# Kernel tuning notes

Measured on AMD Instinct MI355X. Metric: run time of the kernel, lower is better.

Reference implementation:

```python
import jax, jax.numpy as jnp
import numpy as np

BEAMS = 2
DEPTH = 3
NEXP = 4
HID = 128
NCLS = 100
EPS = 1e-5


def _conv(x, w, b):
    y = jax.lax.conv_general_dilated(x, w, (1, 1), 'VALID',
                                     dimension_numbers=('NCHW', 'OIHW', 'NCHW'))
    return y + b.reshape(1, -1, 1, 1)


def _bn(x, g, b):
    # training-mode batch norm over (N, H, W) per channel
    m = jnp.mean(x, axis=(0, 2, 3), keepdims=True)
    v = jnp.var(x, axis=(0, 2, 3), keepdims=True)
    return (x - m) * jax.lax.rsqrt(v + EPS) * g.reshape(1, -1, 1, 1) + b.reshape(1, -1, 1, 1)


def _pool(x):
    return jax.lax.reduce_window(x, 0.0, jax.lax.add, (1, 1, 2, 2), (1, 1, 2, 2), 'VALID') * 0.25


def _backbone(x, blocks):
    h = x
    for (w, b, g, bb) in blocks:  # 3 fixed conv blocks
        h = _pool(jax.nn.relu(_bn(_conv(h, w, b), g, bb)))
    return h.reshape(h.shape[0], -1)  # [B, 128]


def _routed_mlp(h, trajectories, expert_W, expert_b):
    # h: [N, 128] with N = B*BEAMS; trajectories: [DEPTH, B, BEAMS, NEXP]
    N = h.shape[0]
    for d in range(DEPTH):
        ops = trajectories[d].reshape(N, NEXP)
        sel = jnp.argmax(ops, axis=1)                              # per-sample expert id
        all_out = jnp.einsum('nd,eod->neo', h, expert_W) + expert_b[None]  # [N, NEXP, 128]
        out = jnp.take_along_axis(all_out, sel[:, None, None], axis=1)[:, 0, :]
        mx = jnp.max(ops, axis=1, keepdims=True)
        out = out + mx - jax.lax.stop_gradient(mx)                 # straight-through router tie
        if d != DEPTH - 1:
            out = jax.nn.relu(out)
        h = out
    return h


def setup_inputs() -> dict:
    key = jax.random.key(0)
    ks = jax.random.split(key, 12)
    B = 2048
    x = jax.random.normal(ks[0], (B, 3, 32, 32), jnp.float32)
    trajectories = jax.random.uniform(ks[1], (DEPTH, B, BEAMS, NEXP), jnp.float32)
    score_values = jax.random.normal(ks[2], (B, BEAMS), jnp.float32)
    # conv blocks
    cw1 = jax.random.normal(ks[3], (32, 3, 3, 3), jnp.float32) * 0.1
    cb1 = jnp.zeros((32,), jnp.float32)
    g1 = jnp.ones((32,), jnp.float32)
    bb1 = jnp.zeros((32,), jnp.float32)
    cw2 = jax.random.normal(ks[4], (32, 32, 3, 3), jnp.float32) * 0.06
    cb2 = jnp.zeros((32,), jnp.float32)
    g2 = jnp.ones((32,), jnp.float32)
    bb2 = jnp.zeros((32,), jnp.float32)
    cw3 = jax.random.normal(ks[5], (32, 32, 3, 3), jnp.float32) * 0.06
    cb3 = jnp.zeros((32,), jnp.float32)
    g3 = jnp.ones((32,), jnp.float32)
    bb3 = jnp.zeros((32,), jnp.float32)
    # experts: 3 Linear(128,128) + Identity (eye weight, zero bias)
    eW = jax.random.normal(ks[6], (3, HID, HID), jnp.float32) * 0.05
    expert_W = jnp.concatenate([eW, jnp.eye(HID, dtype=jnp.float32)[None]], axis=0)  # [4,128,128]
    eb = jax.random.normal(ks[7], (3, HID), jnp.float32) * 0.01
    expert_b = jnp.concatenate([eb, jnp.zeros((1, HID), jnp.float32)], axis=0)       # [4,128]
    out_W = jax.random.normal(ks[8], (NCLS, HID), jnp.float32) * 0.05
    out_b = jnp.zeros((NCLS,), jnp.float32)
    return dict(x=x, trajectories=trajectories, score_values=score_values,
                cw1=cw1, cb1=cb1, g1=g1, bb1=bb1,
                cw2=cw2, cb2=cb2, g2=g2, bb2=bb2,
                cw3=cw3, cb3=cb3, g3=g3, bb3=bb3,
                expert_W=expert_W, expert_b=expert_b, out_W=out_W, out_b=out_b)


def reference(x, trajectories, score_values,
              cw1, cb1, g1, bb1, cw2, cb2, g2, bb2, cw3, cb3, g3, bb3,
              expert_W, expert_b, out_W, out_b):
    blocks = [(cw1, cb1, g1, bb1), (cw2, cb2, g2, bb2), (cw3, cb3, g3, bb3)]
    h0 = _backbone(x, blocks)                       # [B, 128]
    h = jnp.repeat(h0, BEAMS, axis=0)               # [B*BEAMS, 128], sample-major like torch expand+view
    h = _routed_mlp(h, trajectories, expert_W, expert_b)
    preds = h @ out_W.T + out_b                     # [B*BEAMS, 100]
    logp = jax.nn.log_softmax(preds, axis=1)
    return (logp, score_values)
```

## Files before the change

### kernel.cpp

```cpp
#include <hip/hip_runtime.h>
#include <math.h>

typedef unsigned short us;
typedef short s16x8 __attribute__((ext_vector_type(8)));
typedef float f32x4 __attribute__((ext_vector_type(4)));

#define EPSV 1e-5f

static __device__ inline us f2bf(float f) {
  union { float f; unsigned u; } v; v.f = f;
  unsigned r = v.u + 0x7fffu + ((v.u >> 16) & 1u);
  return (us)(r >> 16);
}
static __device__ inline unsigned cvtpk(float lo, float hi) {
  unsigned r;
  asm("v_cvt_pk_bf16_f32 %0, %1, %2" : "=v"(r) : "v"(lo), "v"(hi));
  return r;
}
static __device__ inline us f2bf1(float f) { return (us)cvtpk(f, 0.f); }
static __device__ inline float bflo(unsigned u) { return __uint_as_float(u << 16); }
static __device__ inline float bfhi(unsigned u) { return __uint_as_float(u & 0xffff0000u); }

union AU { s16x8 v; us e[8]; };

__global__ __launch_bounds__(256) void prep_weights(
    const float* __restrict__ w1, const float* __restrict__ w2,
    const float* __restrict__ w3, const float* __restrict__ eW,
    const float* __restrict__ oW,
    us* __restrict__ wt1L, us* __restrict__ wt1Lb,
    us* __restrict__ wt2L, us* __restrict__ wt3L,
    us* __restrict__ ewB, us* __restrict__ owB) {
  const int gtid = blockIdx.x * 256 + threadIdx.x;
  const int G = gridDim.x * 256;
  for (int i = gtid; i < 1280; i += G) {
    const int oc = i / 40, k = i % 40, t = k >> 2, c = k & 3;
    wt1L[i] = (t < 9 && c < 3) ? f2bf(w1[oc * 27 + c * 9 + t]) : (us)0;
    wt1Lb[i] = (k < 3) ? f2bf(w1[oc * 27 + k * 9 + 8]) : (us)0;
  }
  for (int i = gtid; i < 11520; i += G) {
    const int row = i / 40, col = i % 40;
    const int tap = row >> 5, oc = row & 31;
    wt2L[i] = (col < 32) ? f2bf(w2[oc * 288 + col * 9 + tap]) : (us)0;
    wt3L[i] = (col < 32) ? f2bf(w3[oc * 288 + col * 9 + tap]) : (us)0;
  }
  for (int i = gtid; i < 49152; i += G) ewB[i] = f2bf(eW[i]);
  for (int i = gtid; i < 14336; i += G) {
    const int cls = i >> 7;
    owB[i] = (cls < 100) ? f2bf(oW[cls * 128 + (i & 127)]) : (us)0;
  }
}

__global__ __launch_bounds__(256) void finalize_stats(
    const float* __restrict__ part, const float* __restrict__ g,
    const float* __restrict__ bb, float cnt, float* __restrict__ stats) {
  __shared__ float redS[256], redQ[256];
  const int ch = blockIdx.x, tid = threadIdx.x;
  const float* ps = part + (size_t)ch * 2048;
  const float* pq = part + (size_t)(32 + ch) * 2048;
  float s = 0.f, q = 0.f;
  for (int i = tid; i < 2048; i += 256) { s += ps[i]; q += pq[i]; }
  redS[tid] = s; redQ[tid] = q;
  __syncthreads();
  for (int off = 128; off; off >>= 1) {
    if (tid < off) { redS[tid] += redS[tid + off]; redQ[tid] += redQ[tid + off]; }
    __syncthreads();
  }
  if (tid == 0) {
    const float mean = redS[0] / cnt;
    const float var = redQ[0] / cnt - mean * mean;
    const float sc = g[ch] * rsqrtf(var + EPSV);
    stats[ch] = sc;
    stats[32 + ch] = bb[ch] - mean * sc;
  }
}

static __device__ inline void stage_x_cminor(const float* xp, us* xsb4, int tid) {
#pragma unroll
  for (int k = 0; k < 4; ++k) {
    const int p = tid + k * 256;
    const unsigned lo = cvtpk(xp[p], xp[1024 + p]);
    const unsigned hi = cvtpk(xp[2048 + p], 0.f);
    *(uint2*)&xsb4[p * 4] = make_uint2(lo, hi);
  }
}

static __device__ inline void build_tbl1(us* tbl, int tid) {
  for (int i = tid; i < 928; i += 256) {
    us v = 0;
    if (i < 900) {
      const int w = i >> 2, e = i & 3;
      v = (us)((((2 * (w / 15) + (e >> 1)) * 32 + 2 * (w % 15) + (e & 1))) * 4);
    }
    tbl[i] = v;
  }
}

__global__ __launch_bounds__(256, 4) void conv1_stats(
    const float* __restrict__ x, const us* __restrict__ wt1L,
    const us* __restrict__ wt1Lb, const float* __restrict__ cb,
    float* __restrict__ part1) {
  __shared__ __align__(16) us xsb4[4096];
  __shared__ us tbl1[928];
  __shared__ float csum[32], css[32];
  const int n = blockIdx.x, tid = threadIdx.x;
  const int wave = tid >> 6, lane = tid & 63, row16 = lane & 15, kg = lane >> 4;
  stage_x_cminor(x + (size_t)n * 3072, xsb4, tid);
  build_tbl1(tbl1, tid);
  if (tid < 32) { csum[tid] = 0.f; css[tid] = 0.f; }
  __syncthreads();
  const int t0 = 2 * kg, t1 = 2 * kg + 1;
  const int toff0 = ((t0 / 3) * 32 + t0 % 3) * 4;
  const int toff1 = ((t1 / 3) * 32 + t1 % 3) * 4;
  const s16x8 wf0 = *(const s16x8*)&wt1L[row16 * 40 + kg * 8];
  const s16x8 wf1 = *(const s16x8*)&wt1L[(16 + row16) * 40 + kg * 8];
  const s16x8 wb0 = *(const s16x8*)&wt1Lb[row16 * 40 + kg * 8];
  const s16x8 wb1 = *(const s16x8*)&wt1Lb[(16 + row16) * 40 + kg * 8];
  const float bias0 = cb[row16], bias1 = cb[16 + row16];
  AU a2;
#pragma unroll
  for (int j = 0; j < 8; ++j) a2.e[j] = 0;
  float s0 = 0.f, ss0 = 0.f, s1 = 0.f, ss1 = 0.f;
  for (int mt = wave; mt < 57; mt += 4) {
    const int pixA = mt * 16 + row16;
    const int boff = tbl1[pixA];
    AU a;
    *(uint2*)&a.e[0] = *(const uint2*)&xsb4[boff + toff0];
    *(uint2*)&a.e[4] = *(const uint2*)&xsb4[boff + toff1];
    if (kg == 0) *(uint2*)&a2.e[0] = *(const uint2*)&xsb4[boff + 264];
    f32x4 acc0 = {bias0, bias0, bias0, bias0};
    f32x4 acc1 = {bias1, bias1, bias1, bias1};
    acc0 = __builtin_amdgcn_mfma_f32_16x16x32_bf16(a.v, wf0, acc0, 0, 0, 0);
    acc0 = __builtin_amdgcn_mfma_f32_16x16x32_bf16(a2.v, wb0, acc0, 0, 0, 0);
    acc1 = __builtin_amdgcn_mfma_f32_16x16x32_bf16(a.v, wf1, acc1, 0, 0, 0);
    acc1 = __builtin_amdgcn_mfma_f32_16x16x32_bf16(a2.v, wb1, acc1, 0, 0, 0);
#pragma unroll
    for (int r = 0; r < 4; ++r) {
      const int pix = mt * 16 + kg * 4 + r;
      if (pix < 900) {
        s0 += acc0[r]; ss0 += acc0[r] * acc0[r];
        s1 += acc1[r]; ss1 += acc1[r] * acc1[r];
      }
    }
  }
  s0 += __shfl_down(s0, 32); s0 += __shfl_down(s0, 16);
  ss0 += __shfl_down(ss0, 32); ss0 += __shfl_down(ss0, 16);
  s1 += __shfl_down(s1, 32); s1 += __shfl_down(s1, 16);
  ss1 += __shfl_down(ss1, 32); ss1 += __shfl_down(ss1, 16);
  if (lane < 16) {
    atomicAdd(&csum[row16], s0); atomicAdd(&css[row16], ss0);
    atomicAdd(&csum[16 + row16], s1); atomicAdd(&css[16 + row16], ss1);
  }
  __syncthreads();
  if (tid < 32) {
    part1[tid * 2048 + n] = csum[tid];
    part1[(32 + tid) * 2048 + n] = css[tid];
  }
}

__global__ __launch_bounds__(256, 4) void conv1_apply_conv2_stats(
    const float* __restrict__ x, const us* __restrict__ wt1L,
    const us* __restrict__ wt1Lb, const float* __restrict__ cb1,
    const float* __restrict__ stats1,
    const us* __restrict__ wt2L, const float* __restrict__ cb2,
    float* __restrict__ part2, us* __restrict__ y2s) {
  __shared__ __align__(16) us xsb4[4096];
  __shared__ __align__(16) us p1b[9000];
  __shared__ us tbl1[928];
  __shared__ us tbl2[176];
  __shared__ float scS[32], shS[32], csum[32], css[32];
  const int n = blockIdx.x, tid = threadIdx.x;
  const int wave = tid >> 6, lane = tid & 63, row16 = lane & 15, kg = lane >> 4;
  stage_x_cminor(x + (size_t)n * 3072, xsb4, tid);
  build_tbl1(tbl1, tid);
  if (tid < 176) {
    us v = 0;
    const int q = tid;
    if (q < 144) {
      const int w = q >> 2, e = q & 3;
      v = (us)((2 * (w / 6) + (e >> 1)) * 15 + 2 * (w % 6) + (e & 1));
    } else if (q < 169) {
      const int r = q - 144;
      v = (us)((r < 13) ? (12 * 15 + r) : ((r - 13) * 15 + 12));
    }
    tbl2[tid] = v;
  }
  if (tid < 32) {
    scS[tid] = stats1[tid]; shS[tid] = stats1[32 + tid];
    csum[tid] = 0.f; css[tid] = 0.f;
  }
  __syncthreads();
  {
    const int t0 = 2 * kg, t1 = 2 * kg + 1;
    const int toff0 = ((t0 / 3) * 32 + t0 % 3) * 4;
    const int toff1 = ((t1 / 3) * 32 + t1 % 3) * 4;
    const s16x8 wf0 = *(const s16x8*)&wt1L[row16 * 40 + kg * 8];
    const s16x8 wf1 = *(const s16x8*)&wt1L[(16 + row16) * 40 + kg * 8];
    const s16x8 wb0 = *(const s16x8*)&wt1Lb[row16 * 40 + kg * 8];
    const s16x8 wb1 = *(const s16x8*)&wt1Lb[(16 + row16) * 40 + kg * 8];
    const float bias0 = cb1[row16], bias1 = cb1[16 + row16];
    const float sc0 = scS[row16], sh0 = shS[row16];
    const float sc1 = scS[16 + row16], sh1 = shS[16 + row16];
    AU a2;
#pragma unroll
    for (int j = 0; j < 8; ++j) a2.e[j] = 0;
    for (int mt = wave; mt < 57; mt += 4) {
      const int pixA = mt * 16 + row16;
      const int boff = tbl1[pixA];
      AU a;
      *(uint2*)&a.e[0] = *(const uint2*)&xsb4[boff + toff0];
      *(uint2*)&a.e[4] = *(const uint2*)&xsb4[boff + toff1];
      if (kg == 0) *(uint2*)&a2.e[0] = *(const uint2*)&xsb4[boff + 264];
      f32x4 acc0 = {bias0, bias0, bias0, bias0};
      f32x4 acc1 = {bias1, bias1, bias1, bias1};
      acc0 = __builtin_amdgcn_mfma_f32_16x16x32_bf16(a.v, wf0, acc0, 0, 0, 0);
      acc0 = __builtin_amdgcn_mfma_f32_16x16x32_bf16(a2.v, wb0, acc0, 0, 0, 0);
      acc1 = __builtin_amdgcn_mfma_f32_16x16x32_bf16(a.v, wf1, acc1, 0, 0, 0);
      acc1 = __builtin_amdgcn_mfma_f32_16x16x32_bf16(a2.v, wb1, acc1, 0, 0, 0);
      const int w = mt * 4 + kg;
      if (w < 225) {
        float p0 = 0.f, p1v = 0.f;
#pragma unroll
        for (int r = 0; r < 4; ++r) {
          p0 += fmaxf(acc0[r] * sc0 + sh0, 0.f);
          p1v += fmaxf(acc1[r] * sc1 + sh1, 0.f);
        }
        p1b[w * 40 + row16] = f2bf1(p0 * 0.25f);
        p1b[w * 40 + 16 + row16] = f2bf1(p1v * 0.25f);
      }
    }
  }
  __syncthreads();
  int inb[3], mtv[3];
#pragma unroll
  for (int m = 0; m < 3; ++m) {
    const int mt = wave + 4 * m;
    mtv[m] = mt;
    const int q = mt * 16 + row16;
    inb[m] = tbl2[(q < 176) ? q : 0];
  }
  const float b20 = cb2[row16], b21 = cb2[16 + row16];
  f32x4 acc[3][2];
#pragma unroll
  for (int m = 0; m < 3; ++m) {
    acc[m][0] = {b20, b20, b20, b20};
    acc[m][1] = {b21, b21, b21, b21};
  }
#pragma unroll
  for (int tap = 0; tap < 9; ++tap) {
    const int ki = tap / 3, kj = tap % 3;
    const s16x8 wf0 = *(const s16x8*)&wt2L[(tap * 32 + row16) * 40 + kg * 8];
    const s16x8 wf1 = *(const s16x8*)&wt2L[(tap * 32 + 16 + row16) * 40 + kg * 8];
#pragma unroll
    for (int m = 0; m < 3; ++m) {
      if (mtv[m] < 11) {
        const s16x8 a = *(const s16x8*)&p1b[(inb[m] + ki * 15 + kj) * 40 + kg * 8];
        acc[m][0] = __builtin_amdgcn_mfma_f32_16x16x32_bf16(a, wf0, acc[m][0], 0, 0, 0);
        acc[m][1] = __builtin_amdgcn_mfma_f32_16x16x32_bf16(a, wf1, acc[m][1], 0, 0, 0);
      }
    }
  }
  float s0 = 0.f, ss0 = 0.f, s1 = 0.f, ss1 = 0.f;
#pragma unroll
  for (int m = 0; m < 3; ++m) {
    if (mtv[m] < 11) {
      if (mtv[m] < 9) {
        const int w = mtv[m] * 4 + kg;
        uint2 pk0, pk1;
        pk0.x = cvtpk(acc[m][0][0], acc[m][0][1]);
        pk0.y = cvtpk(acc[m][0][2], acc[m][0][3]);
        pk1.x = cvtpk(acc[m][1][0], acc[m][1][1]);
        pk1.y = cvtpk(acc[m][1][2], acc[m][1][3]);
        *(uint2*)(y2s + (((size_t)n * 36 + w) * 32 + row16) * 4) = pk0;
        *(uint2*)(y2s + (((size_t)n * 36 + w) * 32 + 16 + row16) * 4) = pk1;
      }
#pragma unroll
      for (int r = 0; r < 4; ++r) {
        const int q = mtv[m] * 16 + kg * 4 + r;
        if (q < 169) {
          const float u0 = acc[m][0][r], u1 = acc[m][1][r];
          s0 += u0; ss0 += u0 * u0; s1 += u1; ss1 += u1 * u1;
        }
      }
    }
  }
  s0 += __shfl_down(s0, 32); s0 += __shfl_down(s0, 16);
  ss0 += __shfl_down(ss0, 32); ss0 += __shfl_down(ss0, 16);
  s1 += __shfl_down(s1, 32); s1 += __shfl_down(s1, 16);
  ss1 += __shfl_down(ss1, 32); ss1 += __shfl_down(ss1, 16);
  if (lane < 16) {
    atomicAdd(&csum[row16], s0); atomicAdd(&css[row16], ss0);
    atomicAdd(&csum[16 + row16], s1); atomicAdd(&css[16 + row16], ss1);
  }
  __syncthreads();
  if (tid < 32) {
    part2[tid * 2048 + n] = csum[tid];
    part2[(32 + tid) * 2048 + n] = css[tid];
  }
}

__global__ __launch_bounds__(256) void bnpool2_conv3_stats(
    const us* __restrict__ y2s, const float* __restrict__ stats2,
    const us* __restrict__ wt3L, const float* __restrict__ cb3,
    float* __restrict__ part3, us* __restrict__ p2g) {
  __shared__ __align__(16) us p2L[11520];
  __shared__ float scS[32], shS[32], csum[32], css[32];
  const int n0 = blockIdx.x * 8, tid = threadIdx.x;
  const int wave = tid >> 6, lane = tid & 63, row16 = lane & 15, kg = lane >> 4;
  if (tid < 32) {
    scS[tid] = stats2[tid]; shS[tid] = stats2[32 + tid];
    csum[tid] = 0.f; css[tid] = 0.f;
  }
  __syncthreads();
#pragma unroll
  for (int it = 0; it < 36; ++it) {
    const int i = tid + it * 256;
    const int c = i & 31, w = (i >> 5) % 36, s = i / 1152;
    const uint2 v = *(const uint2*)(y2s + (((size_t)(n0 + s) * 36 + w) * 32 + c) * 4);
    const float sc = scS[c], sh = shS[c];
    const float p = fmaxf(bflo(v.x) * sc + sh, 0.f) + fmaxf(bfhi(v.x) * sc + sh, 0.f) +
                    fmaxf(bflo(v.y) * sc + sh, 0.f) + fmaxf(bfhi(v.y) * sc + sh, 0.f);
    const us pb = f2bf1(p * 0.25f);
    p2L[(s * 36 + w) * 40 + c] = pb;
    p2g[((size_t)(n0 + s) * 36 + w) * 32 + c] = pb;
  }
  __syncthreads();
  const int inb3 = (row16 >> 2) * 6 + (row16 & 3);
  const float b30 = cb3[row16], b31 = cb3[16 + row16];
  float s0 = 0.f, ss0 = 0.f, s1 = 0.f, ss1 = 0.f;
#pragma unroll
  for (int si = 0; si < 2; ++si) {
    const int s = wave * 2 + si;
    f32x4 a0 = {b30, b30, b30, b30};
    f32x4 a1 = {b31, b31, b31, b31};
#pragma unroll
    for (int tap = 0; tap < 9; ++tap) {
      const int ki = tap / 3, kj = tap % 3;
      const s16x8 wf0 = *(const s16x8*)&wt3L[(tap * 32 + row16) * 40 + kg * 8];
      const s16x8 wf1 = *(const s16x8*)&wt3L[(tap * 32 + 16 + row16) * 40 + kg * 8];
      const s16x8 a = *(const s16x8*)&p2L[(s * 36 + inb3 + ki * 6 + kj) * 40 + kg * 8];
      a0 = __builtin_amdgcn_mfma_f32_16x16x32_bf16(a, wf0, a0, 0, 0, 0);
      a1 = __builtin_amdgcn_mfma_f32_16x16x32_bf16(a, wf1, a1, 0, 0, 0);
    }
#pragma unroll
    for (int r = 0; r < 4; ++r) {
      s0 += a0[r]; ss0 += a0[r] * a0[r];
      s1 += a1[r]; ss1 += a1[r] * a1[r];
    }
  }
  s0 += __shfl_down(s0, 32); s0 += __shfl_down(s0, 16);
  ss0 += __shfl_down(ss0, 32); ss0 += __shfl_down(ss0, 16);
  s1 += __shfl_down(s1, 32); s1 += __shfl_down(s1, 16);
  ss1 += __shfl_down(ss1, 32); ss1 += __shfl_down(ss1, 16);
  if (lane < 16) {
    atomicAdd(&csum[row16], s0); atomicAdd(&css[row16], ss0);
    atomicAdd(&csum[16 + row16], s1); atomicAdd(&css[16 + row16], ss1);
  }
  __syncthreads();
  if (tid < 32) {
    part3[tid * 2048 + blockIdx.x] = csum[tid];
    part3[(32 + tid) * 2048 + blockIdx.x] = css[tid];
  }
}

__global__ __launch_bounds__(256) void finalize_stats256(
    const float* __restrict__ part, const float* __restrict__ g,
    const float* __restrict__ bb, float cnt, float* __restrict__ stats) {
  __shared__ float redS[256], redQ[256];
  const int ch = blockIdx.x, tid = threadIdx.x;
  const float* ps = part + (size_t)ch * 2048;
  const float* pq = part + (size_t)(32 + ch) * 2048;
  redS[tid] = ps[tid]; redQ[tid] = pq[tid];
  __syncthreads();
  for (int off = 128; off; off >>= 1) {
    if (tid < off) { redS[tid] += redS[tid + off]; redQ[tid] += redQ[tid + off]; }
    __syncthreads();
  }
  if (tid == 0) {
    const float mean = redS[0] / cnt;
    const float var = redQ[0] / cnt - mean * mean;
    const float sc = g[ch] * rsqrtf(var + EPSV);
    stats[ch] = sc;
    stats[32 + ch] = bb[ch] - mean * sc;
  }
}

__global__ __launch_bounds__(64) void conv3_apply_mlp(
    const us* __restrict__ p2g, const us* __restrict__ wt3L,
    const float* __restrict__ cb3, const float* __restrict__ stats3,
    const float* __restrict__ traj,
    const us* __restrict__ ewB, const float* __restrict__ eb,
    const us* __restrict__ owB, const float* __restrict__ ob,
    float* __restrict__ out) {
  __shared__ __align__(16) us p2L[11520];
  __shared__ float h0a[1024];
  __shared__ __align__(16) us ht[16 * 136];
  __shared__ float scS[32], shS[32], ebl[384], obl[112];
  const int lane = threadIdx.x, row16 = lane & 15, kg = lane >> 4;
  const int n0 = blockIdx.x * 8, rbase = blockIdx.x * 16;
  for (int i = lane; i < 1152; i += 64) {
    const int s = i / 144, ci = i - s * 144;
    const uint4 v = ((const uint4*)(p2g + (size_t)n0 * 1152))[i];
    *(uint4*)&p2L[(s * 36 + (ci >> 2)) * 40 + (ci & 3) * 8] = v;
  }
  if (lane < 32) { scS[lane] = stats3[lane]; shS[lane] = stats3[32 + lane]; }
  for (int i = lane; i < 384; i += 64) ebl[i] = eb[i];
  for (int i = lane; i < 112; i += 64) obl[i] = (i < 100) ? ob[i] : 0.f;
  __syncthreads();
  const int wA = row16 >> 2, eA = row16 & 3;
  const int inb3 = (2 * (wA >> 1) + (eA >> 1)) * 6 + 2 * (wA & 1) + (eA & 1);
  const float b30 = cb3[row16], b31 = cb3[16 + row16];
  const float sc0 = scS[row16], sh0 = shS[row16];
  const float sc1 = scS[16 + row16], sh1 = shS[16 + row16];
#pragma unroll
  for (int s = 0; s < 8; ++s) {
    f32x4 a0 = {b30, b30, b30, b30};
    f32x4 a1 = {b31, b31, b31, b31};
#pragma unroll
    for (int tap = 0; tap < 9; ++tap) {
      const int ki = tap / 3, kj = tap % 3;
      const s16x8 wf0 = *(const s16x8*)&wt3L[(tap * 32 + row16) * 40 + kg * 8];
      const s16x8 wf1 = *(const s16x8*)&wt3L[(tap * 32 + 16 + row16) * 40 + kg * 8];
      const s16x8 a = *(const s16x8*)&p2L[(s * 36 + inb3 + ki * 6 + kj) * 40 + kg * 8];
      a0 = __builtin_amdgcn_mfma_f32_16x16x32_bf16(a, wf0, a0, 0, 0, 0);
      a1 = __builtin_amdgcn_mfma_f32_16x16x32_bf16(a, wf1, a1, 0, 0, 0);
    }
    float p0 = 0.f, p1v = 0.f;
#pragma unroll
    for (int r = 0; r < 4; ++r) {
      p0 += fmaxf(a0[r] * sc0 + sh0, 0.f);
      p1v += fmaxf(a1[r] * sc1 + sh1, 0.f);
    }
    h0a[s * 128 + row16 * 4 + kg] = p0 * 0.25f;
    h0a[s * 128 + (16 + row16) * 4 + kg] = p1v * 0.25f;
  }
  __syncthreads();
#pragma unroll
  for (int q = 0; q < 4; ++q) {
    const int u = lane + q * 64;
    const int lr = u >> 4, d8 = (u & 15) * 8;
    const float* hp = &h0a[(lr >> 1) * 128 + d8];
    uint4 p;
    p.x = cvtpk(hp[0], hp[1]); p.y = cvtpk(hp[2], hp[3]);
    p.z = cvtpk(hp[4], hp[5]); p.w = cvtpk(hp[6], hp[7]);
    *(uint4*)&ht[lr * 136 + d8] = p;
  }
  float accv[8][4];
#pragma unroll
  for (int ct = 0; ct < 8; ++ct)
#pragma unroll
    for (int r = 0; r < 4; ++r)
      accv[ct][r] = h0a[((kg * 4 + r) >> 1) * 128 + ct * 16 + row16];
  __syncthreads();
  for (int d = 0; d < 3; ++d) {
    int sel[4];
#pragma unroll
    for (int r = 0; r < 4; ++r) {
      const int rowg = rbase + kg * 4 + r;
      const float4 t4 = *(const float4*)(traj + d * 16384 + rowg * 4);
      int s = 0; float mx = t4.x;
      if (t4.y > mx) { mx = t4.y; s = 1; }
      if (t4.z > mx) { mx = t4.z; s = 2; }
      if (t4.w > mx) { mx = t4.w; s = 3; }
      sel[r] = s;
    }
    s16x8 a[4];
#pragma unroll
    for (int kc = 0; kc < 4; ++kc)
      a[kc] = *(const s16x8*)&ht[row16 * 136 + kc * 32 + kg * 8];
    float newacc[8][4];
#pragma unroll
    for (int ct = 0; ct < 8; ++ct)
#pragma unroll
      for (int r = 0; r < 4; ++r)
        newacc[ct][r] = (sel[r] == 3) ? accv[ct][r] : 0.f;
#pragma unroll
    for (int e = 0; e < 3; ++e) {
#pragma unroll
      for (int ct = 0; ct < 8; ++ct) {
        f32x4 t = {0.f, 0.f, 0.f, 0.f};
#pragma unroll
        for (int kc = 0; kc < 4; ++kc) {
          const s16x8 b = *(const s16x8*)&ewB[(e * 128 + ct * 16 + row16) * 128 + kc * 32 + kg * 8];
          t = __builtin_amdgcn_mfma_f32_16x16x32_bf16(a[kc], b, t, 0, 0, 0);
        }
        const float bias = ebl[e * 128 + ct * 16 + row16];
#pragma unroll
        for (int r = 0; r < 4; ++r)
          if (sel[r] == e) newacc[ct][r] = t[r] + bias;
      }
    }
#pragma unroll
    for (int ct = 0; ct < 8; ++ct)
#pragma unroll
      for (int r = 0; r < 4; ++r) {
        float v = newacc[ct][r];
        if (d < 2) v = fmaxf(v, 0.f);
        accv[ct][r] = v;
        ht[(kg * 4 + r) * 136 + ct * 16 + row16] = f2bf1(v);
      }
  }
  s16x8 a[4];
#pragma unroll
  for (int kc = 0; kc < 4; ++kc)
    a[kc] = *(const s16x8*)&ht[row16 * 136 + kc * 32 + kg * 8];
  float preds[7][4];
#pragma unroll
  for (int ct = 0; ct < 7; ++ct) {
    f32x4 t = {0.f, 0.f, 0.f, 0.f};
#pragma unroll
    for (int kc = 0; kc < 4; ++kc) {
      const s16x8 b = *(const s16x8*)&owB[(ct * 16 + row16) * 128 + kc * 32 + kg * 8];
      t = __builtin_amdgcn_mfma_f32_16x16x32_bf16(a[kc], b, t, 0, 0, 0);
    }
    const float bias = obl[ct * 16 + row16];
#pragma unroll
    for (int r = 0; r < 4; ++r) preds[ct][r] = t[r] + bias;
  }
  const bool v6 = (96 + row16) < 100;
#pragma unroll
  for (int r = 0; r < 4; ++r) {
    float mx = -INFINITY;
#pragma unroll
    for (int ct = 0; ct < 7; ++ct)
      if (ct < 6 || v6) mx = fmaxf(mx, preds[ct][r]);
    mx = fmaxf(mx, __shfl_xor(mx, 1)); mx = fmaxf(mx, __shfl_xor(mx, 2));
    mx = fmaxf(mx, __shfl_xor(mx, 4)); mx = fmaxf(mx, __shfl_xor(mx, 8));
    float s = 0.f;
#pragma unroll
    for (int ct = 0; ct < 7; ++ct)
      if (ct < 6 || v6) s += expf(preds[ct][r] - mx);
    s += __shfl_xor(s, 1); s += __shfl_xor(s, 2);
    s += __shfl_xor(s, 4); s += __shfl_xor(s, 8);
    const float lg = mx + logf(s);
    const int rowg = rbase + kg * 4 + r;
#pragma unroll
    for (int ct = 0; ct < 7; ++ct)
      if (ct < 6 || v6) out[(size_t)rowg * 100 + ct * 16 + row16] = preds[ct][r] - lg;
  }
}

extern "C" void kernel_launch(void* const* d_in, const int* in_sizes, int n_in,
                              void* d_out, int out_size, void* d_ws, size_t ws_size,
                              hipStream_t stream) {
  const float* x     = (const float*)d_in[0];
  const float* traj  = (const float*)d_in[1];
  const float* score = (const float*)d_in[2];
  const float* cw1 = (const float*)d_in[3];
  const float* cb1 = (const float*)d_in[4];
  const float* g1  = (const float*)d_in[5];
  const float* bb1 = (const float*)d_in[6];
  const float* cw2 = (const float*)d_in[7];
  const float* cb2 = (const float*)d_in[8];
  const float* g2  = (const float*)d_in[9];
  const float* bb2 = (const float*)d_in[10];
  const float* cw3 = (const float*)d_in[11];
  const float* cb3 = (const float*)d_in[12];
  const float* g3  = (const float*)d_in[13];
  const float* bb3 = (const float*)d_in[14];
  const float* eW  = (const float*)d_in[15];
  const float* eb  = (const float*)d_in[16];
  const float* oW  = (const float*)d_in[17];
  const float* ob  = (const float*)d_in[18];
  float* out = (float*)d_out;

  char* ws = (char*)d_ws;
  float* stats1 = (float*)ws;
  float* stats2 = (float*)(ws + 256);
  float* stats3 = (float*)(ws + 512);
  us* wt1L  = (us*)(ws + 1024);
  us* wt1Lb = (us*)(ws + 4096);
  us* wt2L  = (us*)(ws + 8192);
  us* wt3L  = (us*)(ws + 8192 + 23040);
  us* ewB   = (us*)(ws + 65536);
  us* owB   = (us*)(ws + 65536 + 98304);
  us* y2s   = (us*)(ws + 262144);
  us* p2g   = (us*)(ws + 262144 + 18874368);
  char* pbase = ws + 262144 + 18874368 + 4718592;
  float* part1 = (float*)pbase;
  float* part2 = (float*)(pbase + 524288);
  float* part3 = (float*)(pbase + 1048576);

  prep_weights<<<64, 256, 0, stream>>>(cw1, cw2, cw3, eW, oW,
                                       wt1L, wt1Lb, wt2L, wt3L, ewB, owB);
  conv1_stats<<<2048, 256, 0, stream>>>(x, wt1L, wt1Lb, cb1, part1);
  finalize_stats<<<32, 256, 0, stream>>>(part1, g1, bb1, 2048.f * 900.f, stats1);
  conv1_apply_conv2_stats<<<2048, 256, 0, stream>>>(x, wt1L, wt1Lb, cb1, stats1,
                                                    wt2L, cb2, part2, y2s);
  finalize_stats<<<32, 256, 0, stream>>>(part2, g2, bb2, 2048.f * 169.f, stats2);
  bnpool2_conv3_stats<<<256, 256, 0, stream>>>(y2s, stats2, wt3L, cb3, part3, p2g);
  finalize_stats256<<<32, 256, 0, stream>>>(part3, g3, bb3, 2048.f * 16.f, stats3);
  conv3_apply_mlp<<<256, 64, 0, stream>>>(p2g, wt3L, cb3, stats3, traj,
                                          ewB, eb, owB, ob, out);
  hipMemcpyAsync(out + 409600, score, 4096 * sizeof(float),
                 hipMemcpyDeviceToDevice, stream);
}
```

Before: 111.3 us.

## Switch conv1 and conv2 to 32x32x16 MFMA tiles with merged weight layout

Conv1 and conv2 now use 32x32x16 bf16 MFMA instead of pairs of 16x16x32 ops. Each lane maps to one output channel, so all 32 channels come from one MFMA. The conv1 weights become a single 48-wide padded layout, and the tenth tap points to a zeroed LDS pad, which removes the extra tail MFMA and the split weight buffer. This cuts MFMA and instruction count and simplifies stats reduction. The trade-off is larger accumulators and a new row mapping for pooling and stores, which must match the 32x32 output layout.

```diff
diff --git a/kernel.cpp b/kernel.cpp
--- a/kernel.cpp
+++ b/kernel.cpp
@@ -4,6 +4,7 @@
 typedef unsigned short us;
 typedef short s16x8 __attribute__((ext_vector_type(8)));
 typedef float f32x4 __attribute__((ext_vector_type(4)));
+typedef float f32x16 __attribute__((ext_vector_type(16)));
 
 #define EPSV 1e-5f
 
@@ -27,15 +28,13 @@
     const float* __restrict__ w1, const float* __restrict__ w2,
     const float* __restrict__ w3, const float* __restrict__ eW,
     const float* __restrict__ oW,
-    us* __restrict__ wt1L, us* __restrict__ wt1Lb,
-    us* __restrict__ wt2L, us* __restrict__ wt3L,
+    us* __restrict__ wt1n, us* __restrict__ wt2L, us* __restrict__ wt3L,
     us* __restrict__ ewB, us* __restrict__ owB) {
   const int gtid = blockIdx.x * 256 + threadIdx.x;
   const int G = gridDim.x * 256;
-  for (int i = gtid; i < 1280; i += G) {
-    const int oc = i / 40, k = i % 40, t = k >> 2, c = k & 3;
-    wt1L[i] = (t < 9 && c < 3) ? f2bf(w1[oc * 27 + c * 9 + t]) : (us)0;
-    wt1Lb[i] = (k < 3) ? f2bf(w1[oc * 27 + k * 9 + 8]) : (us)0;
+  for (int i = gtid; i < 1536; i += G) {
+    const int oc = i / 48, k = i % 48, t = k >> 2, c = k & 3;
+    wt1n[i] = (t < 9 && c < 3) ? f2bf(w1[oc * 27 + c * 9 + t]) : (us)0;
   }
   for (int i = gtid; i < 11520; i += G) {
     const int row = i / 40, col = i % 40;
@@ -82,6 +81,7 @@
     const unsigned hi = cvtpk(xp[2048 + p], 0.f);
     *(uint2*)&xsb4[p * 4] = make_uint2(lo, hi);
   }
+  if (tid < 16) *(uint4*)&xsb4[4096 + tid * 8] = make_uint4(0, 0, 0, 0);
 }
 
 static __device__ inline void build_tbl1(us* tbl, int tid) {
@@ -95,61 +95,54 @@
   }
 }
 
+static __device__ inline int tapoff(int t) {
+  return (t < 9) ? (((t / 3) * 32 + t % 3) * 4) : 4096;
+}
+
 __global__ __launch_bounds__(256, 4) void conv1_stats(
-    const float* __restrict__ x, const us* __restrict__ wt1L,
-    const us* __restrict__ wt1Lb, const float* __restrict__ cb,
-    float* __restrict__ part1) {
-  __shared__ __align__(16) us xsb4[4096];
+    const float* __restrict__ x, const us* __restrict__ wt1n,
+    const float* __restrict__ cb, float* __restrict__ part1) {
+  __shared__ __align__(16) us xsb4[4224];
   __shared__ us tbl1[928];
   __shared__ float csum[32], css[32];
   const int n = blockIdx.x, tid = threadIdx.x;
-  const int wave = tid >> 6, lane = tid & 63, row16 = lane & 15, kg = lane >> 4;
+  const int wave = tid >> 6, lane = tid & 63, oc = lane & 31, hi = lane >> 5;
   stage_x_cminor(x + (size_t)n * 3072, xsb4, tid);
   build_tbl1(tbl1, tid);
   if (tid < 32) { csum[tid] = 0.f; css[tid] = 0.f; }
   __syncthreads();
-  const int t0 = 2 * kg, t1 = 2 * kg + 1;
-  const int toff0 = ((t0 / 3) * 32 + t0 % 3) * 4;
-  const int toff1 = ((t1 / 3) * 32 + t1 % 3) * 4;
-  const s16x8 wf0 = *(const s16x8*)&wt1L[row16 * 40 + kg * 8];
-  const s16x8 wf1 = *(const s16x8*)&wt1L[(16 + row16) * 40 + kg * 8];
-  const s16x8 wb0 = *(const s16x8*)&wt1Lb[row16 * 40 + kg * 8];
-  const s16x8 wb1 = *(const s16x8*)&wt1Lb[(16 + row16) * 40 + kg * 8];
-  const float bias0 = cb[row16], bias1 = cb[16 + row16];
-  AU a2;
-#pragma unroll
-  for (int j = 0; j < 8; ++j) a2.e[j] = 0;
-  float s0 = 0.f, ss0 = 0.f, s1 = 0.f, ss1 = 0.f;
-  for (int mt = wave; mt < 57; mt += 4) {
-    const int pixA = mt * 16 + row16;
-    const int boff = tbl1[pixA];
-    AU a;
-    *(uint2*)&a.e[0] = *(const uint2*)&xsb4[boff + toff0];
-    *(uint2*)&a.e[4] = *(const uint2*)&xsb4[boff + toff1];
-    if (kg == 0) *(uint2*)&a2.e[0] = *(const uint2*)&xsb4[boff + 264];
-    f32x4 acc0 = {bias0, bias0, bias0, bias0};
-    f32x4 acc1 = {bias1, bias1, bias1, bias1};
-    acc0 = __builtin_amdgcn_mfma_f32_16x16x32_bf16(a.v, wf0, acc0, 0, 0, 0);
-    acc0 = __builtin_amdgcn_mfma_f32_16x16x32_bf16(a2.v, wb0, acc0, 0, 0, 0);
-    acc1 = __builtin_amdgcn_mfma_f32_16x16x32_bf16(a.v, wf1, acc1, 0, 0, 0);
-    acc1 = __builtin_amdgcn_mfma_f32_16x16x32_bf16(a2.v, wb1, acc1, 0, 0, 0);
-#pragma unroll
-    for (int r = 0; r < 4; ++r) {
-      const int pix = mt * 16 + kg * 4 + r;
-      if (pix < 900) {
-        s0 += acc0[r]; ss0 += acc0[r] * acc0[r];
-        s1 += acc1[r]; ss1 += acc1[r] * acc1[r];
-      }
-    }
-  }
-  s0 += __shfl_down(s0, 32); s0 += __shfl_down(s0, 16);
-  ss0 += __shfl_down(ss0, 32); ss0 += __shfl_down(ss0, 16);
-  s1 += __shfl_down(s1, 32); s1 += __shfl_down(s1, 16);
-  ss1 += __shfl_down(ss1, 32); ss1 += __shfl_down(ss1, 16);
-  if (lane < 16) {
-    atomicAdd(&csum[row16], s0); atomicAdd(&css[row16], ss0);
-    atomicAdd(&csum[16 + row16], s1); atomicAdd(&css[16 + row16], ss1);
-  }
+  int tA[3], tB[3];
+#pragma unroll
+  for (int kk = 0; kk < 3; ++kk) {
+    tA[kk] = tapoff(4 * kk + 2 * hi);
+    tB[kk] = tapoff(4 * kk + 2 * hi + 1);
+  }
+  s16x8 wb[3];
+#pragma unroll
+  for (int kk = 0; kk < 3; ++kk)
+    wb[kk] = *(const s16x8*)&wt1n[oc * 48 + kk * 16 + hi * 8];
+  const float bias = cb[oc];
+  float s = 0.f, ss = 0.f;
+  for (int mt = wave; mt < 29; mt += 4) {
+    const int boff = tbl1[mt * 32 + oc + 0 * hi + (lane & 31) - oc];
+    f32x16 acc;
+#pragma unroll
+    for (int r = 0; r < 16; ++r) acc[r] = bias;
+#pragma unroll
+    for (int kk = 0; kk < 3; ++kk) {
+      AU a;
+      *(uint2*)&a.e[0] = *(const uint2*)&xsb4[boff + tA[kk]];
+      *(uint2*)&a.e[4] = *(const uint2*)&xsb4[boff + tB[kk]];
+      acc = __builtin_amdgcn_mfma_f32_32x32x16_bf16(a.v, wb[kk], acc, 0, 0, 0);
+    }
+#pragma unroll
+    for (int reg = 0; reg < 16; ++reg) {
+      const int row = mt * 32 + (reg & 3) + 8 * (reg >> 2) + 4 * hi;
+      if (row < 900) { s += acc[reg]; ss += acc[reg] * acc[reg]; }
+    }
+  }
+  s += __shfl_down(s, 32); ss += __shfl_down(ss, 32);
+  if (lane < 32) { atomicAdd(&csum[oc], s); atomicAdd(&css[oc], ss); }
   __syncthreads();
   if (tid < 32) {
     part1[tid * 2048 + n] = csum[tid];
@@ -158,21 +151,20 @@
 }
 
 __global__ __launch_bounds__(256, 4) void conv1_apply_conv2_stats(
-    const float* __restrict__ x, const us* __restrict__ wt1L,
-    const us* __restrict__ wt1Lb, const float* __restrict__ cb1,
-    const float* __restrict__ stats1,
+    const float* __restrict__ x, const us* __restrict__ wt1n,
+    const float* __restrict__ cb1, const float* __restrict__ stats1,
     const us* __restrict__ wt2L, const float* __restrict__ cb2,
     float* __restrict__ part2, us* __restrict__ y2s) {
-  __shared__ __align__(16) us xsb4[4096];
+  __shared__ __align__(16) us xsb4[4224];
   __shared__ __align__(16) us p1b[9000];
   __shared__ us tbl1[928];
-  __shared__ us tbl2[176];
+  __shared__ us tbl2[192];
   __shared__ float scS[32], shS[32], csum[32], css[32];
   const int n = blockIdx.x, tid = threadIdx.x;
-  const int wave = tid >> 6, lane = tid & 63, row16 = lane & 15, kg = lane >> 4;
+  const int wave = tid >> 6, lane = tid & 63, oc = lane & 31, hi = lane >> 5;
   stage_x_cminor(x + (size_t)n * 3072, xsb4, tid);
   build_tbl1(tbl1, tid);
-  if (tid < 176) {
+  if (tid < 192) {
     us v = 0;
     const int q = tid;
     if (q < 144) {
@@ -190,106 +182,79 @@
   }
   __syncthreads();
   {
-    const int t0 = 2 * kg, t1 = 2 * kg + 1;
-    const int toff0 = ((t0 / 3) * 32 + t0 % 3) * 4;
-    const int toff1 = ((t1 / 3) * 32 + t1 % 3) * 4;
-    const s16x8 wf0 = *(const s16x8*)&wt1L[row16 * 40 + kg * 8];
-    const s16x8 wf1 = *(const s16x8*)&wt1L[(16 + row16) * 40 + kg * 8];
-    const s16x8 wb0 = *(const s16x8*)&wt1Lb[row16 * 40 + kg * 8];
-    const s16x8 wb1 = *(const s16x8*)&wt1Lb[(16 + row16) * 40 + kg * 8];
-    const float bias0 = cb1[row16], bias1 = cb1[16 + row16];
-    const float sc0 = scS[row16], sh0 = shS[row16];
-    const float sc1 = scS[16 + row16], sh1 = shS[16 + row16];
-    AU a2;
-#pragma unroll
-    for (int j = 0; j < 8; ++j) a2.e[j] = 0;
-    for (int mt = wave; mt < 57; mt += 4) {
-      const int pixA = mt * 16 + row16;
-      const int boff = tbl1[pixA];
-      AU a;
-      *(uint2*)&a.e[0] = *(const uint2*)&xsb4[boff + toff0];
-      *(uint2*)&a.e[4] = *(const uint2*)&xsb4[boff + toff1];
-      if (kg == 0) *(uint2*)&a2.e[0] = *(const uint2*)&xsb4[boff + 264];
-      f32x4 acc0 = {bias0, bias0, bias0, bias0};
-      f32x4 acc1 = {bias1, bias1, bias1, bias1};
-      acc0 = __builtin_amdgcn_mfma_f32_16x16x32_bf16(a.v, wf0, acc0, 0, 0, 0);
-      acc0 = __builtin_amdgcn_mfma_f32_16x16x32_bf16(a2.v, wb0, acc0, 0, 0, 0);
-      acc1 = __builtin_amdgcn_mfma_f32_16x16x32_bf16(a.v, wf1, acc1, 0, 0, 0);
-      acc1 = __builtin_amdgcn_mfma_f32_16x16x32_bf16(a2.v, wb1, acc1, 0, 0, 0);
-      const int w = mt * 4 + kg;
-      if (w < 225) {
-        float p0 = 0.f, p1v = 0.f;
-#pragma unroll
-        for (int r = 0; r < 4; ++r) {
-          p0 += fmaxf(acc0[r] * sc0 + sh0, 0.f);
-          p1v += fmaxf(acc1[r] * sc1 + sh1, 0.f);
+    int tA[3], tB[3];
+#pragma unroll
+    for (int kk = 0; kk < 3; ++kk) {
+      tA[kk] = tapoff(4 * kk + 2 * hi);
+      tB[kk] = tapoff(4 * kk + 2 * hi + 1);
+    }
+    s16x8 wb[3];
+#pragma unroll
+    for (int kk = 0; kk < 3; ++kk)
+      wb[kk] = *(const s16x8*)&wt1n[oc * 48 + kk * 16 + hi * 8];
+    const float bias = cb1[oc];
+    const float sc = scS[oc], sh = shS[oc];
+    for (int mt = wave; mt < 29; mt += 4) {
+      const int boff = tbl1[mt * 32 + (lane & 31)];
+      f32x16 acc;
+#pragma unroll
+      for (int r = 0; r < 16; ++r) acc[r] = bias;
+#pragma unroll
+      for (int kk = 0; kk < 3; ++kk) {
+        AU a;
+        *(uint2*)&a.e[0] = *(const uint2*)&xsb4[boff + tA[kk]];
+        *(uint2*)&a.e[4] = *(const uint2*)&xsb4[boff + tB[kk]];
+        acc = __builtin_amdgcn_mfma_f32_32x32x16_bf16(a.v, wb[kk], acc, 0, 0, 0);
+      }
+#pragma unroll
+      for (int q = 0; q < 4; ++q) {
+        const int w = mt * 8 + 2 * q + hi;
+        if (w < 225) {
+          float p = 0.f;
+#pragma unroll
+          for (int r = 0; r < 4; ++r) p += fmaxf(acc[q * 4 + r] * sc + sh, 0.f);
+          p1b[w * 40 + oc] = f2bf1(p * 0.25f);
         }
-        p1b[w * 40 + row16] = f2bf1(p0 * 0.25f);
-        p1b[w * 40 + 16 + row16] = f2bf1(p1v * 0.25f);
-      }
-    }
-  }
-  __syncthreads();
-  int inb[3], mtv[3];
-#pragma unroll
-  for (int m = 0; m < 3; ++m) {
-    const int mt = wave + 4 * m;
-    mtv[m] = mt;
-    const int q = mt * 16 + row16;
-    inb[m] = tbl2[(q < 176) ? q : 0];
-  }
-  const float b20 = cb2[row16], b21 = cb2[16 + row16];
-  f32x4 acc[3][2];
-#pragma unroll
-  for (int m = 0; m < 3; ++m) {
-    acc[m][0] = {b20, b20, b20, b20};
-    acc[m][1] = {b21, b21, b21, b21};
-  }
-#pragma unroll
-  for (int tap = 0; tap < 9; ++tap) {
-    const int ki = tap / 3, kj = tap % 3;
-    const s16x8 wf0 = *(const s16x8*)&wt2L[(tap * 32 + row16) * 40 + kg * 8];
-    const s16x8 wf1 = *(const s16x8*)&wt2L[(tap * 32 + 16 + row16) * 40 + kg * 8];
-#pragma unroll
-    for (int m = 0; m < 3; ++m) {
-      if (mtv[m] < 11) {
-        const s16x8 a = *(const s16x8*)&p1b[(inb[m] + ki * 15 + kj) * 40 + kg * 8];
-        acc[m][0] = __builtin_amdgcn_mfma_f32_16x16x32_bf16(a, wf0, acc[m][0], 0, 0, 0);
-        acc[m][1] = __builtin_amdgcn_mfma_f32_16x16x32_bf16(a, wf1, acc[m][1], 0, 0, 0);
-      }
-    }
-  }
-  float s0 = 0.f, ss0 = 0.f, s1 = 0.f, ss1 = 0.f;
-#pragma unroll
-  for (int m = 0; m < 3; ++m) {
-    if (mtv[m] < 11) {
-      if (mtv[m] < 9) {
-        const int w = mtv[m] * 4 + kg;
-        uint2 pk0, pk1;
-        pk0.x = cvtpk(acc[m][0][0], acc[m][0][1]);
-        pk0.y = cvtpk(acc[m][0][2], acc[m][0][3]);
-        pk1.x = cvtpk(acc[m][1][0], acc[m][1][1]);
-        pk1.y = cvtpk(acc[m][1][2], acc[m][1][3]);
-        *(uint2*)(y2s + (((size_t)n * 36 + w) * 32 + row16) * 4) = pk0;
-        *(uint2*)(y2s + (((size_t)n * 36 + w) * 32 + 16 + row16) * 4) = pk1;
-      }
-#pragma unroll
-      for (int r = 0; r < 4; ++r) {
-        const int q = mtv[m] * 16 + kg * 4 + r;
-        if (q < 169) {
-          const float u0 = acc[m][0][r], u1 = acc[m][1][r];
-          s0 += u0; ss0 += u0 * u0; s1 += u1; ss1 += u1 * u1;
+      }
+    }
+  }
+  __syncthreads();
+  {
+    const float bias2 = cb2[oc];
+    float s = 0.f, ss = 0.f;
+    for (int mt2 = wave; mt2 < 6; mt2 += 4) {
+      const int inb = tbl2[mt2 * 32 + (lane & 31)];
+      f32x16 acc;
+#pragma unroll
+      for (int r = 0; r < 16; ++r) acc[r] = bias2;
+#pragma unroll
+      for (int tap = 0; tap < 9; ++tap) {
+        const int ki = tap / 3, kj = tap % 3;
+#pragma unroll
+        for (int kk = 0; kk < 2; ++kk) {
+          const s16x8 a = *(const s16x8*)&p1b[(inb + ki * 15 + kj) * 40 + kk * 16 + hi * 8];
+          const s16x8 b = *(const s16x8*)&wt2L[(tap * 32 + oc) * 40 + kk * 16 + hi * 8];
+          acc = __builtin_amdgcn_mfma_f32_32x32x16_bf16(a, b, acc, 0, 0, 0);
         }
       }
-    }
-  }
-  s0 += __shfl_down(s0, 32); s0 += __shfl_down(s0, 16);
-  ss0 += __shfl_down(ss0, 32); ss0 += __shfl_down(ss0, 16);
-  s1 += __shfl_down(s1, 32); s1 += __shfl_down(s1, 16);
-  ss1 += __shfl_down(ss1, 32); ss1 += __shfl_down(ss1, 16);
-  if (lane < 16) {
-    atomicAdd(&csum[row16], s0); atomicAdd(&css[row16], ss0);
-    atomicAdd(&csum[16 + row16], s1); atomicAdd(&css[16 + row16], ss1);
+#pragma unroll
+      for (int q = 0; q < 4; ++q) {
+        const int wloc = mt2 * 8 + 2 * q + hi;
+        if (wloc < 36) {
+          uint2 pk;
+          pk.x = cvtpk(acc[q * 4 + 0], acc[q * 4 + 1]);
+          pk.y = cvtpk(acc[q * 4 + 2], acc[q * 4 + 3]);
+          *(uint2*)(y2s + (((size_t)n * 36 + wloc) * 32 + oc) * 4) = pk;
+        }
+      }
+#pragma unroll
+      for (int reg = 0; reg < 16; ++reg) {
+        const int row = mt2 * 32 + (reg & 3) + 8 * (reg >> 2) + 4 * hi;
+        if (row < 169) { s += acc[reg]; ss += acc[reg] * acc[reg]; }
+      }
+    }
+    s += __shfl_down(s, 32); ss += __shfl_down(ss, 32);
+    if (lane < 32) { atomicAdd(&csum[oc], s); atomicAdd(&css[oc], ss); }
   }
   __syncthreads();
   if (tid < 32) {
@@ -567,8 +532,7 @@
   float* stats1 = (float*)ws;
   float* stats2 = (float*)(ws + 256);
   float* stats3 = (float*)(ws + 512);
-  us* wt1L  = (us*)(ws + 1024);
-  us* wt1Lb = (us*)(ws + 4096);
+  us* wt1n  = (us*)(ws + 1024);
   us* wt2L  = (us*)(ws + 8192);
   us* wt3L  = (us*)(ws + 8192 + 23040);
   us* ewB   = (us*)(ws + 65536);
@@ -581,10 +545,10 @@
   float* part3 = (float*)(pbase + 1048576);
 
   prep_weights<<<64, 256, 0, stream>>>(cw1, cw2, cw3, eW, oW,
-                                       wt1L, wt1Lb, wt2L, wt3L, ewB, owB);
-  conv1_stats<<<2048, 256, 0, stream>>>(x, wt1L, wt1Lb, cb1, part1);
+                                       wt1n, wt2L, wt3L, ewB, owB);
+  conv1_stats<<<2048, 256, 0, stream>>>(x, wt1n, cb1, part1);
   finalize_stats<<<32, 256, 0, stream>>>(part1, g1, bb1, 2048.f * 900.f, stats1);
-  conv1_apply_conv2_stats<<<2048, 256, 0, stream>>>(x, wt1L, wt1Lb, cb1, stats1,
+  conv1_apply_conv2_stats<<<2048, 256, 0, stream>>>(x, wt1n, cb1, stats1,
                                                     wt2L, cb2, part2, y2s);
   finalize_stats<<<32, 256, 0, stream>>>(part2, g2, bb2, 2048.f * 169.f, stats2);
   bnpool2_conv3_stats<<<256, 256, 0, stream>>>(y2s, stats2, wt3L, cb3, part3, p2g);
```

Result: faster. 98.65 us (-11.4%).
